# Kernel optimization log

Hardware: AMD Instinct MI355X
Metric: run time of the kernel (lower is better)

## Reference

```python
import jax, jax.numpy as jnp
import numpy as np
import math

B, S, D, H = 2, 2048, 1024, 16
DK = D // H
EPS = 1e-5

def setup_inputs() -> dict:
    key = jax.random.key(0)
    ks = jax.random.split(key, 16)
    s = 0.02
    return {
        'query': jax.random.normal(ks[0], (B, S, D), jnp.float32),
        'key': jax.random.normal(ks[1], (B, S, D), jnp.float32),
        'value': jax.random.normal(ks[2], (B, S, D), jnp.float32),
        'mask': jax.random.randint(ks[3], (B, 1, S, S), 0, 2, jnp.int32),
        'market_context': jax.random.normal(ks[4], (B, D), jnp.float32),
        'Wq': jax.random.normal(ks[5], (D, D), jnp.float32) * s,
        'bq': jnp.zeros((D,), jnp.float32),
        'Wk': jax.random.normal(ks[6], (D, D), jnp.float32) * s,
        'bk': jnp.zeros((D,), jnp.float32),
        'Wv': jax.random.normal(ks[7], (D, D), jnp.float32) * s,
        'bv': jnp.zeros((D,), jnp.float32),
        'Wo': jax.random.normal(ks[8], (D, D), jnp.float32) * s,
        'bo': jnp.zeros((D,), jnp.float32),
        'Wc': jax.random.normal(ks[9], (D, D), jnp.float32) * s,
        'bc': jnp.zeros((D,), jnp.float32),
        'ln_g': jnp.ones((D,), jnp.float32),
        'ln_b': jnp.zeros((D,), jnp.float32),
    }

def reference(query, key, value, mask, market_context,
              Wq, bq, Wk, bk, Wv, bv, Wo, bo, Wc, bc, ln_g, ln_b):
    b, s, d = query.shape
    # QKV projections -> [B, H, S, DK]
    Q = (query @ Wq + bq).reshape(b, s, H, DK).transpose(0, 2, 1, 3)
    K = (key @ Wk + bk).reshape(b, s, H, DK).transpose(0, 2, 1, 3)
    V = (value @ Wv + bv).reshape(b, s, H, DK).transpose(0, 2, 1, 3)
    # market context -> per-head bias added to K (broadcast over sequence)
    ctx = (market_context @ Wc + bc).reshape(b, H, DK)
    K = K + ctx[:, :, None, :]
    scores = jnp.einsum('bhqd,bhkd->bhqk', Q, K) / math.sqrt(DK)
    scores = jnp.where(mask == 0, jnp.float32(-1e9), scores)
    attn = jax.nn.softmax(scores, axis=-1)  # dropout is identity in eval
    ctx2 = jnp.einsum('bhqk,bhkd->bhqd', attn, V)
    ctx2 = ctx2.transpose(0, 2, 1, 3).reshape(b, s, d)
    out = ctx2 @ Wo + bo
    x = out + query
    mu = jnp.mean(x, axis=-1, keepdims=True)
    var = jnp.mean((x - mu) ** 2, axis=-1, keepdims=True)
    return (x - mu) * jax.lax.rsqrt(var + EPS) * ln_g + ln_b
```

## Files before the change

### kernel.cpp

```cpp
#include <hip/hip_runtime.h>
#include <cstdint>

typedef unsigned short u16;
typedef __attribute__((ext_vector_type(8))) short s16x8;
typedef __attribute__((ext_vector_type(8))) unsigned short u16x8;
typedef __attribute__((ext_vector_type(4))) float f32x4;
typedef __attribute__((ext_vector_type(16))) float f32x16;
typedef __attribute__((ext_vector_type(2))) unsigned uint2v;
typedef __attribute__((ext_vector_type(4))) unsigned uint4v;

#define CKF 0.18033688011f

__device__ inline u16 f2bf(float f){
  union { float f; uint32_t u; } v; v.f = f;
  uint32_t r = v.u + 0x7fffu + ((v.u >> 16) & 1u);
  return (u16)(r >> 16);
}

__device__ inline f32x4 mfma16(s16x8 a, s16x8 b, f32x4 c){
  return __builtin_amdgcn_mfma_f32_16x16x32_bf16(a, b, c, 0, 0, 0);
}
__device__ inline f32x16 mfma32(s16x8 a, s16x8 b, f32x16 c){
  return __builtin_amdgcn_mfma_f32_32x32x16_bf16(a, b, c, 0, 0, 0);
}
__device__ inline unsigned cvtpk(float a, float b){
  unsigned r;
  asm("v_cvt_pk_bf16_f32 %0, %1, %2" : "=v"(r) : "v"(a), "v"(b));
  return r;
}
__device__ inline float exp2a(float x){
  float r;
  asm("v_exp_f32 %0, %1" : "=v"(r) : "v"(x));
  return r;
}
__device__ inline void glds16(const u16* g, u16* l){
  __builtin_amdgcn_global_load_lds((const __attribute__((address_space(1))) void*)g,
                                   (__attribute__((address_space(3))) void*)l, 16, 0, 0);
}
__device__ inline void glds4(const unsigned* g, unsigned* l){
  __builtin_amdgcn_global_load_lds((const __attribute__((address_space(1))) void*)g,
                                   (__attribute__((address_space(3))) void*)l, 4, 0, 0);
}

struct PrepParams {
  const float* q; const float* k; const float* v;
  const int* mask; const float* mc;
  const float* W0; const float* W1; const float* W2; const float* W3;
  const float* Wc;
  u16* qo; u16* ko; u16* vo;
  u16* T0; u16* T1; u16* T2; u16* T3;
  unsigned* bits; float* part;
};

__global__ __launch_bounds__(256) void prep_kernel(PrepParams PP){
  __shared__ float shf[1056];
  int blk = blockIdx.x, tid = threadIdx.x;
  if (blk < 6144){
    int byy = blk >> 11, bxx = blk & 2047;
    const float* src = (byy == 0) ? PP.q : (byy == 1) ? PP.k : PP.v;
    u16* dst = (byy == 0) ? PP.qo : (byy == 1) ? PP.ko : PP.vo;
    size_t i = ((size_t)bxx * 256 + tid) * 8;
    float4 a = *(const float4*)(src + i);
    float4 b = *(const float4*)(src + i + 4);
    u16x8 o = { f2bf(a.x), f2bf(a.y), f2bf(a.z), f2bf(a.w),
                f2bf(b.x), f2bf(b.y), f2bf(b.z), f2bf(b.w) };
    *(u16x8*)(dst + i) = o;
  } else if (blk < 10240){
    int idx = blk - 6144;
    int bxx = idx & 31, byy = (idx >> 5) & 31, bzz = idx >> 10;
    const float* W = (bzz == 0) ? PP.W0 : (bzz == 1) ? PP.W1 : (bzz == 2) ? PP.W2 : PP.W3;
    u16* T = (bzz == 0) ? PP.T0 : (bzz == 1) ? PP.T1 : (bzz == 2) ? PP.T2 : PP.T3;
    float (*t)[33] = (float(*)[33])shf;
    int n0 = bxx * 32, k0 = byy * 32;
    int tx = tid & 31, ty = tid >> 5;
    #pragma unroll
    for (int j = 0; j < 4; j++)
      t[ty + j*8][tx] = W[(size_t)(k0 + ty + j*8) * 1024 + n0 + tx];
    __syncthreads();
    #pragma unroll
    for (int j = 0; j < 4; j++)
      T[(size_t)(n0 + ty + j*8) * 1024 + k0 + tx] = f2bf(t[tx][ty + j*8]);
  } else if (blk < 43008){
    size_t i = (size_t)(blk - 10240) * 256 + tid;
    int v = PP.mask[i];
    unsigned long long bal = __ballot(v != 0);
    int lane = tid & 63;
    if (lane == 0)       PP.bits[i >> 5] = (unsigned)bal;
    else if (lane == 32) PP.bits[i >> 5] = (unsigned)(bal >> 32);
  } else {
    int slice = blk - 43008;
    int k0 = slice * 64;
    float4 a0 = {0.f,0.f,0.f,0.f}, a1 = {0.f,0.f,0.f,0.f};
    const float* wp = PP.Wc + (size_t)k0 * 1024 + tid * 4;
    #pragma unroll 8
    for (int k = 0; k < 64; k++){
      float4 wv = *(const float4*)(wp + (size_t)k * 1024);
      float m0 = PP.mc[k0 + k], m1 = PP.mc[1024 + k0 + k];
      a0.x += m0 * wv.x; a0.y += m0 * wv.y; a0.z += m0 * wv.z; a0.w += m0 * wv.w;
      a1.x += m1 * wv.x; a1.y += m1 * wv.y; a1.z += m1 * wv.z; a1.w += m1 * wv.w;
    }
    *(float4*)(PP.part + ((size_t)slice * 2 + 0) * 1024 + tid * 4) = a0;
    *(float4*)(PP.part + ((size_t)slice * 2 + 1) * 1024 + tid * 4) = a1;
  }
}

__global__ __launch_bounds__(256) void ctxred_kernel(const float* __restrict__ part,
                                                     const float* __restrict__ bc,
                                                     float* __restrict__ ctx){
  int b = blockIdx.x, tid = threadIdx.x;
  float4 s = *(const float4*)(bc + tid * 4);
  #pragma unroll 4
  for (int sl = 0; sl < 16; sl++){
    float4 p = *(const float4*)(part + ((size_t)sl * 2 + b) * 1024 + tid * 4);
    s.x += p.x; s.y += p.y; s.z += p.z; s.w += p.w;
  }
  *(float4*)(ctx + (size_t)b * 1024 + tid * 4) = s;
}

struct GemmParams {
  const u16* A0; const u16* A1; const u16* A2; const u16* A3;
  const u16* W0; const u16* W1; const u16* W2; const u16* W3;
  const float* b0; const float* b1; const float* b2;
  const float* ctx;
  u16* outQ; u16* outK; u16* outV; float* outX0; float* outX1;
  int which;
};

__global__ __launch_bounds__(256, 2) void gemm_kernel(GemmParams P){
  int o = blockIdx.x + (blockIdx.y << 2) + (blockIdx.z << 7);
  int xcd = o & 7, j = o >> 3;
  int by = xcd + ((j & 3) << 3);
  int bx = (j >> 2) & 3;
  int bz = j >> 4;

  int z, kbase, nkt;
  const u16* A; const u16* W;
  if (P.which < 0){
    z = bz; kbase = 0; nkt = 32;
    if (z == 0){ A = P.A0; W = P.W0; }
    else if (z == 1){ A = P.A1; W = P.W1; }
    else { A = P.A2; W = P.W2; }
  } else {
    z = 3; kbase = bz * 512; nkt = 16;
    A = P.A3; W = P.W3;
  }
  int m0 = by * 128, n0 = bx * 256;
  __shared__ __align__(16) u16 sm[24576];
  int tid = threadIdx.x, lane = tid & 63, w = tid >> 6;
  int li = lane & 15, lq = lane >> 4;
  int wm = w >> 1, wn = w & 1;
  f32x4 zero = {0.f, 0.f, 0.f, 0.f};
  f32x4 acc[4][8];
  #pragma unroll
  for (int i = 0; i < 4; i++)
    #pragma unroll
    for (int jj = 0; jj < 8; jj++) acc[i][jj] = zero;

  int scolS = ((lane & 3) ^ ((lane >> 3) & 3)) << 3;
  int rowS = w * 16 + (lane >> 2);
  const u16* aS0 = A + (size_t)(m0 + rowS) * 1024 + kbase + scolS;
  const u16* aS1 = aS0 + (size_t)64 * 1024;
  const u16* bS0 = W + (size_t)(n0 + rowS) * 1024 + kbase + scolS;
  const u16* bS1 = bS0 + (size_t)64 * 1024;
  const u16* bS2 = bS0 + (size_t)128 * 1024;
  const u16* bS3 = bS0 + (size_t)192 * 1024;
  int d0 = (w * 64) * 8, d1 = (256 + w * 64) * 8;
  int d2 = (512 + w * 64) * 8, d3 = (768 + w * 64) * 8;

  int aOff[4], bOff[8];
  #pragma unroll
  for (int mb = 0; mb < 4; mb++){
    int row = wm * 64 + mb * 16 + li;
    aOff[mb] = (row * 32 + ((lq ^ ((row >> 1) & 3)) << 3)) * 2;
  }
  #pragma unroll
  for (int nb = 0; nb < 8; nb++){
    int row = wn * 128 + nb * 16 + li;
    bOff[nb] = 8192 + (row * 32 + ((lq ^ ((row >> 1) & 3)) << 3)) * 2;
  }

  auto STAGE = [&](int ct){
    u16* Ab = &sm[ct * 12288];
    u16* Bb = &sm[ct * 12288 + 4096];
    glds16(aS0, Ab + d0);
    glds16(aS1, Ab + d1);
    glds16(bS0, Bb + d0);
    glds16(bS1, Bb + d1);
    glds16(bS2, Bb + d2);
    glds16(bS3, Bb + d3);
  };
  auto ADV = [&](){ aS0 += 32; aS1 += 32; bS0 += 32; bS1 += 32; bS2 += 32; bS3 += 32; };

  auto KITER = [&](int kt, int ct){
    __builtin_amdgcn_s_barrier();
    if (kt + 1 < nkt){
      STAGE(ct ^ 1); ADV();
      asm volatile("s_waitcnt vmcnt(6)" ::: "memory");
    } else {
      asm volatile("s_waitcnt vmcnt(0)" ::: "memory");
    }
    __builtin_amdgcn_sched_barrier(0);
    __builtin_amdgcn_s_barrier();
    const char* base = (const char*)sm + ct * 24576;
    s16x8 af[4], bfr[8];
    #pragma unroll
    for (int mb = 0; mb < 4; mb++) af[mb] = *(const s16x8*)(base + aOff[mb]);
    #pragma unroll
    for (int nb = 0; nb < 8; nb++) bfr[nb] = *(const s16x8*)(base + bOff[nb]);
    __builtin_amdgcn_s_setprio(1);
    #pragma unroll
    for (int mb = 0; mb < 4; mb++)
      #pragma unroll
      for (int nb = 0; nb < 8; nb++)
        acc[mb][nb] = mfma16(af[mb], bfr[nb], acc[mb][nb]);
    __builtin_amdgcn_s_setprio(0);
  };

  STAGE(0); ADV();
  for (int kt = 0; kt < nkt; kt += 2){
    KITER(kt, 0);
    KITER(kt + 1, 1);
  }

  if (z == 2){
    const float* bias = P.b2;
    int bq_ = m0 >> 11, srow0 = m0 & 2047;
    u16* Ot = sm;
    #pragma unroll
    for (int h2 = 0; h2 < 2; h2++){
      __syncthreads();
      if (wn == h2){
        #pragma unroll
        for (int mb = 0; mb < 4; mb++){
          #pragma unroll
          for (int nb = 0; nb < 8; nb++){
            int cl = nb * 16 + li;
            int rowB = wm * 64 + mb * 16 + lq * 4;
            float bcol = bias[n0 + h2 * 128 + cl];
            unsigned p01 = cvtpk(acc[mb][nb][0] + bcol, acc[mb][nb][1] + bcol);
            unsigned p23 = cvtpk(acc[mb][nb][2] + bcol, acc[mb][nb][3] + bcol);
            int ba = cl * 256 + ((rowB * 2) ^ ((cl & 7) << 4));
            *(unsigned*)((char*)Ot + ba) = p01;
            *(unsigned*)((char*)Ot + ba + 4) = p23;
          }
        }
      }
      __syncthreads();
      #pragma unroll
      for (int i = 0; i < 8; i++){
        int u = i * 256 + tid;
        int cl = u >> 4, sc = u & 15;
        int ba = cl * 256 + ((sc * 16) ^ ((cl & 7) << 4));
        u16x8 vv = *(const u16x8*)((char*)Ot + ba);
        *(u16x8*)(P.outV + (((size_t)(bq_ * 1024 + n0 + h2 * 128 + cl)) << 11) + srow0 + sc * 8) = vv;
      }
    }
    return;
  }

  if (z == 3){
    float* Xo = (kbase == 0) ? P.outX0 : P.outX1;
    #pragma unroll
    for (int mb = 0; mb < 4; mb++){
      #pragma unroll
      for (int nb = 0; nb < 8; nb++){
        int col = n0 + wn * 128 + nb * 16 + li;
        #pragma unroll
        for (int r = 0; r < 4; r++){
          int row = m0 + wm * 64 + mb * 16 + lq * 4 + r;
          Xo[(size_t)row * 1024 + col] = acc[mb][nb][r];
        }
      }
    }
    return;
  }

  const float* bias = (z == 0) ? P.b0 : P.b1;
  #pragma unroll
  for (int mb = 0; mb < 4; mb++){
    #pragma unroll
    for (int nb = 0; nb < 8; nb++){
      int colL = wn * 128 + nb * 16 + li; int col = n0 + colL;
      float bcol = bias[col];
      #pragma unroll
      for (int r = 0; r < 4; r++){
        int row = m0 + wm * 64 + mb * 16 + lq * 4 + r;
        float v = acc[mb][nb][r] + bcol;
        if (z == 0){
          P.outQ[(size_t)row * 1024 + col] = f2bf(v * CKF);
        } else {
          v += P.ctx[(size_t)(row >> 11) * 1024 + col];
          P.outK[(size_t)row * 1024 + col] = f2bf(v);
        }
      }
    }
  }
}

__global__ __launch_bounds__(256) void attn_kernel(
    const u16* __restrict__ Qg, const u16* __restrict__ Kg, const u16* __restrict__ Vtg,
    const unsigned* __restrict__ mbits, u16* __restrict__ ctx2){
  __shared__ __align__(16) u16 arena[17408];
  int tid = threadIdx.x, lane = tid & 63, w = tid >> 6;
  int l31 = lane & 31, hi = lane >> 5;
  int r7 = l31 & 7;
  int orig = blockIdx.x + (blockIdx.y << 4);
  int swz = (orig & 7) * 64 + (orig >> 3);
  int q0 = (swz & 15) * 128, bh = swz >> 4, b = bh >> 4, h = bh & 15;

  s16x8 qf[4];
  {
    const u16* qp = Qg + (size_t)(b * 2048 + q0 + w * 32 + l31) * 1024 + h * 64 + hi * 8;
    #pragma unroll
    for (int ks = 0; ks < 4; ks++)
      qf[ks] = *(const s16x8*)(qp + ks * 16);
  }
  s16x8 onesf;
  #pragma unroll
  for (int e = 0; e < 8; e++) onesf[e] = (short)0x3F80;
  f32x16 ZERO;
  #pragma unroll
  for (int r = 0; r < 16; r++) ZERO[r] = 0.f;

  int scolS = ((lane & 7) ^ (lane >> 3)) << 3;
  int rowS = w * 16 + (lane >> 3);
  const u16* kS0 = Kg + (size_t)(b * 2048 + rowS) * 1024 + h * 64 + scolS;
  const u16* kS1 = kS0 + (size_t)8 * 1024;
  const u16* vS0 = Vtg + (((size_t)(bh * 64 + rowS)) << 11) + scolS;
  const u16* vS1 = vS0 + ((size_t)8 << 11);
  int um = w * 64 + lane;
  const unsigned* mS = mbits + (size_t)(b * 2048 + q0 + (um >> 1)) * 64 + (um & 1);
  int kD0 = w * 1024, kD1 = w * 1024 + 512;

  int qr = w * 32 + l31;
  int koff[2][4], voff[2][4];
  #pragma unroll
  for (int jj = 0; jj < 2; jj++)
    #pragma unroll
    for (int ks = 0; ks < 4; ks++){
      koff[jj][ks] = ((jj * 32 + l31) * 64 + (((ks * 2 + hi) ^ r7) << 3)) * 2;
      voff[jj][ks] = 8192 + ((jj * 32 + l31) * 64 + (((ks * 2 + hi) ^ r7) << 3)) * 2;
    }
  int mB = 32768 + qr * 8;

  auto STAGE = [&](int ct){
    u16* dst = &arena[ct * 8192];
    glds16(kS0, dst + kD0);
    glds16(kS1, dst + kD1);
    glds16(vS0, dst + 4096 + kD0);
    glds16(vS1, dst + 4096 + kD1);
    glds4(mS, (unsigned*)&arena[16384] + ct * 256 + w * 64);
  };
  auto ADV = [&](){
    kS0 += (size_t)64 * 1024; kS1 += (size_t)64 * 1024;
    vS0 += 64; vS1 += 64; mS += 2;
  };

  f32x16 accO[2], accS;
  #pragma unroll
  for (int d = 0; d < 2; d++) accO[d] = ZERO;
  accS = ZERO;

  STAGE(0); ADV();

  auto ITER = [&](int t, int ct){
    __builtin_amdgcn_s_barrier();
    if (t < 31){
      STAGE(ct ^ 1); ADV();
      asm volatile("s_waitcnt vmcnt(5)" ::: "memory");
    } else {
      asm volatile("s_waitcnt vmcnt(0)" ::: "memory");
    }
    __builtin_amdgcn_sched_barrier(0);
    __builtin_amdgcn_s_barrier();
    const char* base = (const char*)arena + ct * 16384;

    f32x16 S[2];
    __builtin_amdgcn_s_setprio(1);
    #pragma unroll
    for (int jj = 0; jj < 2; jj++){
      S[jj] = ZERO;
      #pragma unroll
      for (int ks = 0; ks < 4; ks++){
        s16x8 kf = *(const s16x8*)(base + koff[jj][ks]);
        S[jj] = mfma32(kf, qf[ks], S[jj]);
      }
    }
    __builtin_amdgcn_s_setprio(0);

    uint2v mw = *(const uint2v*)((const char*)arena + ct * 1024 + mB);
    unsigned mh0 = mw[0] >> (hi << 2), mh1 = mw[1] >> (hi << 2);
    #pragma unroll
    for (int jj = 0; jj < 2; jj++){
      unsigned mh = jj ? mh1 : mh0;
      #pragma unroll
      for (int rg = 0; rg < 16; rg++){
        int pos = (rg & 3) + ((rg >> 2) << 3);
        float pv = exp2a(S[jj][rg]);
        S[jj][rg] = ((mh >> pos) & 1u) ? pv : 0.f;
      }
    }

    s16x8 pf[4];
    #pragma unroll
    for (int jj = 0; jj < 2; jj++){
      #pragma unroll
      for (int hs = 0; hs < 2; hs++){
        int rb = hs * 8;
        unsigned A0 = cvtpk(S[jj][rb + 0], S[jj][rb + 1]);
        unsigned A1 = cvtpk(S[jj][rb + 2], S[jj][rb + 3]);
        unsigned B0 = cvtpk(S[jj][rb + 4], S[jj][rb + 5]);
        unsigned B1 = cvtpk(S[jj][rb + 6], S[jj][rb + 7]);
        uint2v r01 = __builtin_amdgcn_permlane32_swap(A0, B0, false, false);
        uint2v r23 = __builtin_amdgcn_permlane32_swap(A1, B1, false, false);
        uint4v uu = { r01[0], r23[0], r01[1], r23[1] };
        pf[jj * 2 + hs] = *(s16x8*)&uu;
      }
    }
    __builtin_amdgcn_s_setprio(1);
    #pragma unroll
    for (int c = 0; c < 4; c++){
      #pragma unroll
      for (int dh = 0; dh < 2; dh++){
        s16x8 vf = *(const s16x8*)(base + voff[dh][c]);
        accO[dh] = mfma32(vf, pf[c], accO[dh]);
      }
      accS = mfma32(onesf, pf[c], accS);
    }
    __builtin_amdgcn_s_setprio(0);
  };

  for (int t = 0; t < 32; t += 2){
    ITER(t, 0);
    ITER(t + 1, 1);
  }

  __syncthreads();
  float lsum = accS[0];
  float inv = 1.f / lsum;
  u16* Ot = arena;
  #pragma unroll
  for (int dh = 0; dh < 2; dh++){
    #pragma unroll
    for (int rg = 0; rg < 16; rg += 2){
      int dk = dh * 32 + (rg & 3) + ((rg >> 2) << 3) + (hi << 2);
      unsigned pk = cvtpk(accO[dh][rg] * inv, accO[dh][rg + 1] * inv);
      *(unsigned*)&Ot[qr * 64 + (((dk >> 3) ^ (qr & 7)) << 3) + (dk & 7)] = pk;
    }
  }
  __syncthreads();
  #pragma unroll
  for (int i = 0; i < 4; i++){
    int u = i * 256 + tid, row = u >> 3, slot = u & 7;
    u16x8 vv = *(const u16x8*)&Ot[row * 64 + ((slot ^ (row & 7)) << 3)];
    *(u16x8*)(ctx2 + (size_t)(b * 2048 + q0 + row) * 1024 + h * 64 + slot * 8) = vv;
  }
}

__global__ __launch_bounds__(256) void ln_kernel(const float* __restrict__ X0,
                                                 const float* __restrict__ X1,
                                                 const float* __restrict__ qres,
                                                 const float* __restrict__ bo,
                                                 const float* __restrict__ g,
                                                 const float* __restrict__ bb,
                                                 float* __restrict__ out){
  size_t row = blockIdx.x;
  int tid = threadIdx.x;
  float4 a = *(const float4*)(X0 + row * 1024 + tid * 4);
  float4 c = *(const float4*)(X1 + row * 1024 + tid * 4);
  float4 q = *(const float4*)(qres + row * 1024 + tid * 4);
  float4 bv = *(const float4*)(bo + tid * 4);
  float4 v;
  v.x = a.x + c.x + q.x + bv.x;
  v.y = a.y + c.y + q.y + bv.y;
  v.z = a.z + c.z + q.z + bv.z;
  v.w = a.w + c.w + q.w + bv.w;
  float s = v.x + v.y + v.z + v.w;
  float s2 = v.x*v.x + v.y*v.y + v.z*v.z + v.w*v.w;
  #pragma unroll
  for (int o = 1; o < 64; o <<= 1){
    s += __shfl_xor(s, o, 64);
    s2 += __shfl_xor(s2, o, 64);
  }
  __shared__ float rs[4], rs2[4];
  int w = tid >> 6;
  if ((tid & 63) == 0){ rs[w] = s; rs2[w] = s2; }
  __syncthreads();
  s = rs[0] + rs[1] + rs[2] + rs[3];
  s2 = rs2[0] + rs2[1] + rs2[2] + rs2[3];
  float mu = s * (1.f / 1024.f);
  float var = s2 * (1.f / 1024.f) - mu * mu;
  float rstd = rsqrtf(var + 1e-5f);
  float4 gg = *(const float4*)(g + tid * 4);
  float4 bt = *(const float4*)(bb + tid * 4);
  float4 o;
  o.x = (v.x - mu) * rstd * gg.x + bt.x;
  o.y = (v.y - mu) * rstd * gg.y + bt.y;
  o.z = (v.z - mu) * rstd * gg.z + bt.z;
  o.w = (v.w - mu) * rstd * gg.w + bt.w;
  *(float4*)(out + row * 1024 + tid * 4) = o;
}

extern "C" void kernel_launch(void* const* d_in, const int* in_sizes, int n_in,
                              void* d_out, int out_size, void* d_ws, size_t ws_size,
                              hipStream_t stream){
  const float* query = (const float*)d_in[0];
  const float* key_  = (const float*)d_in[1];
  const float* value = (const float*)d_in[2];
  const int*   mask  = (const int*)d_in[3];
  const float* mc    = (const float*)d_in[4];
  const float* Wq = (const float*)d_in[5];  const float* bq = (const float*)d_in[6];
  const float* Wk = (const float*)d_in[7];  const float* bk = (const float*)d_in[8];
  const float* Wv = (const float*)d_in[9];  const float* bv = (const float*)d_in[10];
  const float* Wo = (const float*)d_in[11]; const float* bo = (const float*)d_in[12];
  const float* Wc = (const float*)d_in[13]; const float* bc = (const float*)d_in[14];
  const float* lng = (const float*)d_in[15]; const float* lnb = (const float*)d_in[16];
  float* outp = (float*)d_out;
  uint8_t* ws = (uint8_t*)d_ws;
  const size_t MB = (size_t)1 << 20;
  if (ws_size < 58 * MB) return;

  u16* q_bf = (u16*)(ws + 0);
  u16* k_bf = (u16*)(ws + 8 * MB);
  u16* v_bf = (u16*)(ws + 16 * MB);
  float* X0 = (float*)(ws + 8 * MB);
  u16* Qb   = (u16*)(ws + 24 * MB);
  u16* Kb   = (u16*)(ws + 32 * MB);
  float* X1 = (float*)(ws + 32 * MB);
  u16* Vt   = (u16*)(ws + 40 * MB);
  u16* Wqt  = (u16*)(ws + 48 * MB);
  u16* Wkt  = (u16*)(ws + 50 * MB);
  u16* Wvt  = (u16*)(ws + 52 * MB);
  u16* Wot  = (u16*)(ws + 54 * MB);
  unsigned* mbits = (unsigned*)(ws + 56 * MB);
  float* ctxf = (float*)(ws + 57 * MB);
  float* ctxpart = (float*)(ws + 57 * MB + 65536);
  u16* ctx2 = q_bf;

  PrepParams PP;
  PP.q = query; PP.k = key_; PP.v = value; PP.mask = mask; PP.mc = mc;
  PP.W0 = Wq; PP.W1 = Wk; PP.W2 = Wv; PP.W3 = Wo; PP.Wc = Wc;
  PP.qo = q_bf; PP.ko = k_bf; PP.vo = v_bf;
  PP.T0 = Wqt; PP.T1 = Wkt; PP.T2 = Wvt; PP.T3 = Wot;
  PP.bits = mbits; PP.part = ctxpart;
  prep_kernel<<<43024, 256, 0, stream>>>(PP);

  ctxred_kernel<<<2, 256, 0, stream>>>(ctxpart, bc, ctxf);

  GemmParams gp;
  gp.A0 = q_bf; gp.A1 = k_bf; gp.A2 = v_bf; gp.A3 = ctx2;
  gp.W0 = Wqt;  gp.W1 = Wkt;  gp.W2 = Wvt;  gp.W3 = Wot;
  gp.b0 = bq;   gp.b1 = bk;   gp.b2 = bv;
  gp.ctx = ctxf;
  gp.outQ = Qb; gp.outK = Kb; gp.outV = Vt; gp.outX0 = X0; gp.outX1 = X1;
  gp.which = -1;
  gemm_kernel<<<dim3(4, 32, 3), 256, 0, stream>>>(gp);

  attn_kernel<<<dim3(16, 32), 256, 0, stream>>>(Qb, Kb, Vt, mbits, ctx2);

  gp.which = 3;
  gemm_kernel<<<dim3(4, 32, 2), 256, 0, stream>>>(gp);

  ln_kernel<<<4096, 256, 0, stream>>>(X0, X1, query, bo, lng, lnb, outp);
}
```

Measured before the change: 161.1 us.

## Halve GEMM N-tile and split attention key range across two wave groups

The GEMM tile shrinks from 128x256 to 128x128, doubling the grid (8x32 blocks per z) and cutting LDS and accumulator use per block. The attention kernel goes to 512 threads: two wave groups each process half of the key sequence with their own double-buffered LDS staging. Their partial outputs and row sums are then merged through LDS before normalization. This targets occupancy and latency hiding on the many CUs, in exchange for more global traffic in the GEMMs, a larger LDS footprint in attention and an extra reduction step.

```diff
diff --git a/kernel.cpp b/kernel.cpp
--- a/kernel.cpp
+++ b/kernel.cpp
@@ -126,12 +126,12 @@
   int which;
 };
 
-__global__ __launch_bounds__(256, 2) void gemm_kernel(GemmParams P){
-  int o = blockIdx.x + (blockIdx.y << 2) + (blockIdx.z << 7);
+__global__ __launch_bounds__(256) void gemm_kernel(GemmParams P){
+  int o = blockIdx.x + (blockIdx.y << 3) + (blockIdx.z << 8);
   int xcd = o & 7, j = o >> 3;
   int by = xcd + ((j & 3) << 3);
-  int bx = (j >> 2) & 3;
-  int bz = j >> 4;
+  int bx = (j >> 2) & 7;
+  int bz = j >> 5;
 
   int z, kbase, nkt;
   const u16* A; const u16* W;
@@ -144,74 +144,69 @@
     z = 3; kbase = bz * 512; nkt = 16;
     A = P.A3; W = P.W3;
   }
-  int m0 = by * 128, n0 = bx * 256;
-  __shared__ __align__(16) u16 sm[24576];
+  int m0 = by * 128, n0 = bx * 128;
+  __shared__ __align__(16) u16 sm[16384];
   int tid = threadIdx.x, lane = tid & 63, w = tid >> 6;
   int li = lane & 15, lq = lane >> 4;
   int wm = w >> 1, wn = w & 1;
   f32x4 zero = {0.f, 0.f, 0.f, 0.f};
-  f32x4 acc[4][8];
+  f32x4 acc[4][4];
   #pragma unroll
   for (int i = 0; i < 4; i++)
     #pragma unroll
-    for (int jj = 0; jj < 8; jj++) acc[i][jj] = zero;
+    for (int jj = 0; jj < 4; jj++) acc[i][jj] = zero;
 
   int scolS = ((lane & 3) ^ ((lane >> 3) & 3)) << 3;
-  int rowS = w * 16 + (lane >> 2);
-  const u16* aS0 = A + (size_t)(m0 + rowS) * 1024 + kbase + scolS;
+  int row0 = w * 16 + (lane >> 2);
+  const u16* aS0 = A + (size_t)(m0 + row0) * 1024 + kbase + scolS;
   const u16* aS1 = aS0 + (size_t)64 * 1024;
-  const u16* bS0 = W + (size_t)(n0 + rowS) * 1024 + kbase + scolS;
+  const u16* bS0 = W + (size_t)(n0 + row0) * 1024 + kbase + scolS;
   const u16* bS1 = bS0 + (size_t)64 * 1024;
-  const u16* bS2 = bS0 + (size_t)128 * 1024;
-  const u16* bS3 = bS0 + (size_t)192 * 1024;
-  int d0 = (w * 64) * 8, d1 = (256 + w * 64) * 8;
-  int d2 = (512 + w * 64) * 8, d3 = (768 + w * 64) * 8;
-
-  int aOff[4], bOff[8];
+  int aD0 = (w * 64) * 8, aD1 = (256 + w * 64) * 8;
+
+  int aOff[4], bOff[4];
   #pragma unroll
   for (int mb = 0; mb < 4; mb++){
     int row = wm * 64 + mb * 16 + li;
     aOff[mb] = (row * 32 + ((lq ^ ((row >> 1) & 3)) << 3)) * 2;
   }
   #pragma unroll
-  for (int nb = 0; nb < 8; nb++){
-    int row = wn * 128 + nb * 16 + li;
+  for (int nb = 0; nb < 4; nb++){
+    int row = wn * 64 + nb * 16 + li;
     bOff[nb] = 8192 + (row * 32 + ((lq ^ ((row >> 1) & 3)) << 3)) * 2;
   }
 
   auto STAGE = [&](int ct){
-    u16* Ab = &sm[ct * 12288];
-    u16* Bb = &sm[ct * 12288 + 4096];
-    glds16(aS0, Ab + d0);
-    glds16(aS1, Ab + d1);
-    glds16(bS0, Bb + d0);
-    glds16(bS1, Bb + d1);
-    glds16(bS2, Bb + d2);
-    glds16(bS3, Bb + d3);
+    u16* Ab = &sm[ct * 8192];
+    u16* Bb = &sm[ct * 8192 + 4096];
+    glds16(aS0, Ab + aD0);
+    glds16(aS1, Ab + aD1);
+    glds16(bS0, Bb + aD0);
+    glds16(bS1, Bb + aD1);
   };
-  auto ADV = [&](){ aS0 += 32; aS1 += 32; bS0 += 32; bS1 += 32; bS2 += 32; bS3 += 32; };
+  auto ADV = [&](){ aS0 += 32; aS1 += 32; bS0 += 32; bS1 += 32; };
 
   auto KITER = [&](int kt, int ct){
     __builtin_amdgcn_s_barrier();
     if (kt + 1 < nkt){
       STAGE(ct ^ 1); ADV();
-      asm volatile("s_waitcnt vmcnt(6)" ::: "memory");
+      asm volatile("s_waitcnt vmcnt(4)" ::: "memory");
     } else {
       asm volatile("s_waitcnt vmcnt(0)" ::: "memory");
     }
     __builtin_amdgcn_sched_barrier(0);
     __builtin_amdgcn_s_barrier();
-    const char* base = (const char*)sm + ct * 24576;
-    s16x8 af[4], bfr[8];
+    const char* base = (const char*)sm + ct * 16384;
+    s16x8 af[4], bfr[4];
     #pragma unroll
     for (int mb = 0; mb < 4; mb++) af[mb] = *(const s16x8*)(base + aOff[mb]);
     #pragma unroll
-    for (int nb = 0; nb < 8; nb++) bfr[nb] = *(const s16x8*)(base + bOff[nb]);
+    for (int nb = 0; nb < 4; nb++) bfr[nb] = *(const s16x8*)(base + bOff[nb]);
     __builtin_amdgcn_s_setprio(1);
     #pragma unroll
     for (int mb = 0; mb < 4; mb++)
       #pragma unroll
-      for (int nb = 0; nb < 8; nb++)
+      for (int nb = 0; nb < 4; nb++)
         acc[mb][nb] = mfma16(af[mb], bfr[nb], acc[mb][nb]);
     __builtin_amdgcn_s_setprio(0);
   };
@@ -224,36 +219,31 @@
 
   if (z == 2){
     const float* bias = P.b2;
+    __syncthreads();
+    u16* Ot = sm;
+    #pragma unroll
+    for (int mb = 0; mb < 4; mb++){
+      #pragma unroll
+      for (int nb = 0; nb < 4; nb++){
+        int colL = wn * 64 + nb * 16 + li;
+        int rowB = wm * 64 + mb * 16 + lq * 4;
+        float bcol = bias[n0 + colL];
+        unsigned p01 = cvtpk(acc[mb][nb][0] + bcol, acc[mb][nb][1] + bcol);
+        unsigned p23 = cvtpk(acc[mb][nb][2] + bcol, acc[mb][nb][3] + bcol);
+        int ba = colL * 256 + ((rowB * 2) ^ ((colL & 7) << 4));
+        *(unsigned*)((char*)Ot + ba) = p01;
+        *(unsigned*)((char*)Ot + ba + 4) = p23;
+      }
+    }
+    __syncthreads();
     int bq_ = m0 >> 11, srow0 = m0 & 2047;
-    u16* Ot = sm;
-    #pragma unroll
-    for (int h2 = 0; h2 < 2; h2++){
-      __syncthreads();
-      if (wn == h2){
-        #pragma unroll
-        for (int mb = 0; mb < 4; mb++){
-          #pragma unroll
-          for (int nb = 0; nb < 8; nb++){
-            int cl = nb * 16 + li;
-            int rowB = wm * 64 + mb * 16 + lq * 4;
-            float bcol = bias[n0 + h2 * 128 + cl];
-            unsigned p01 = cvtpk(acc[mb][nb][0] + bcol, acc[mb][nb][1] + bcol);
-            unsigned p23 = cvtpk(acc[mb][nb][2] + bcol, acc[mb][nb][3] + bcol);
-            int ba = cl * 256 + ((rowB * 2) ^ ((cl & 7) << 4));
-            *(unsigned*)((char*)Ot + ba) = p01;
-            *(unsigned*)((char*)Ot + ba + 4) = p23;
-          }
-        }
-      }
-      __syncthreads();
-      #pragma unroll
-      for (int i = 0; i < 8; i++){
-        int u = i * 256 + tid;
-        int cl = u >> 4, sc = u & 15;
-        int ba = cl * 256 + ((sc * 16) ^ ((cl & 7) << 4));
-        u16x8 vv = *(const u16x8*)((char*)Ot + ba);
-        *(u16x8*)(P.outV + (((size_t)(bq_ * 1024 + n0 + h2 * 128 + cl)) << 11) + srow0 + sc * 8) = vv;
-      }
+    #pragma unroll
+    for (int i = 0; i < 8; i++){
+      int u = i * 256 + tid;
+      int colL = u >> 4, sc = u & 15;
+      int ba = colL * 256 + ((sc * 16) ^ ((colL & 7) << 4));
+      u16x8 vv = *(const u16x8*)((char*)Ot + ba);
+      *(u16x8*)(P.outV + (((size_t)(bq_ * 1024 + n0 + colL)) << 11) + srow0 + sc * 8) = vv;
     }
     return;
   }
@@ -263,8 +253,8 @@
     #pragma unroll
     for (int mb = 0; mb < 4; mb++){
       #pragma unroll
-      for (int nb = 0; nb < 8; nb++){
-        int col = n0 + wn * 128 + nb * 16 + li;
+      for (int nb = 0; nb < 4; nb++){
+        int col = n0 + wn * 64 + nb * 16 + li;
         #pragma unroll
         for (int r = 0; r < 4; r++){
           int row = m0 + wm * 64 + mb * 16 + lq * 4 + r;
@@ -279,8 +269,8 @@
   #pragma unroll
   for (int mb = 0; mb < 4; mb++){
     #pragma unroll
-    for (int nb = 0; nb < 8; nb++){
-      int colL = wn * 128 + nb * 16 + li; int col = n0 + colL;
+    for (int nb = 0; nb < 4; nb++){
+      int colL = wn * 64 + nb * 16 + li; int col = n0 + colL;
       float bcol = bias[col];
       #pragma unroll
       for (int r = 0; r < 4; r++){
@@ -297,20 +287,22 @@
   }
 }
 
-__global__ __launch_bounds__(256) void attn_kernel(
+__global__ __launch_bounds__(512) void attn_kernel(
     const u16* __restrict__ Qg, const u16* __restrict__ Kg, const u16* __restrict__ Vtg,
     const unsigned* __restrict__ mbits, u16* __restrict__ ctx2){
-  __shared__ __align__(16) u16 arena[17408];
+  __shared__ __align__(16) u16 arena[36864];
   int tid = threadIdx.x, lane = tid & 63, w = tid >> 6;
+  int qw = w & 3, p = w >> 2;
   int l31 = lane & 31, hi = lane >> 5;
   int r7 = l31 & 7;
   int orig = blockIdx.x + (blockIdx.y << 4);
   int swz = (orig & 7) * 64 + (orig >> 3);
   int q0 = (swz & 15) * 128, bh = swz >> 4, b = bh >> 4, h = bh & 15;
+  int qr = qw * 32 + l31;
 
   s16x8 qf[4];
   {
-    const u16* qp = Qg + (size_t)(b * 2048 + q0 + w * 32 + l31) * 1024 + h * 64 + hi * 8;
+    const u16* qp = Qg + (size_t)(b * 2048 + q0 + qr) * 1024 + h * 64 + hi * 8;
     #pragma unroll
     for (int ks = 0; ks < 4; ks++)
       qf[ks] = *(const s16x8*)(qp + ks * 16);
@@ -323,16 +315,15 @@
   for (int r = 0; r < 16; r++) ZERO[r] = 0.f;
 
   int scolS = ((lane & 7) ^ (lane >> 3)) << 3;
-  int rowS = w * 16 + (lane >> 3);
-  const u16* kS0 = Kg + (size_t)(b * 2048 + rowS) * 1024 + h * 64 + scolS;
+  int rowS = qw * 16 + (lane >> 3);
+  const u16* kS0 = Kg + (size_t)(b * 2048 + p * 64 + rowS) * 1024 + h * 64 + scolS;
   const u16* kS1 = kS0 + (size_t)8 * 1024;
-  const u16* vS0 = Vtg + (((size_t)(bh * 64 + rowS)) << 11) + scolS;
+  const u16* vS0 = Vtg + (((size_t)(bh * 64 + rowS)) << 11) + p * 64 + scolS;
   const u16* vS1 = vS0 + ((size_t)8 << 11);
-  int um = w * 64 + lane;
-  const unsigned* mS = mbits + (size_t)(b * 2048 + q0 + (um >> 1)) * 64 + (um & 1);
-  int kD0 = w * 1024, kD1 = w * 1024 + 512;
-
-  int qr = w * 32 + l31;
+  int um = qw * 64 + lane;
+  const unsigned* mS = mbits + (size_t)(b * 2048 + q0 + (um >> 1)) * 64 + p * 2 + (um & 1);
+  int kD0 = qw * 1024, kD1 = qw * 1024 + 512;
+
   int koff[2][4], voff[2][4];
   #pragma unroll
   for (int jj = 0; jj < 2; jj++)
@@ -341,19 +332,20 @@
       koff[jj][ks] = ((jj * 32 + l31) * 64 + (((ks * 2 + hi) ^ r7) << 3)) * 2;
       voff[jj][ks] = 8192 + ((jj * 32 + l31) * 64 + (((ks * 2 + hi) ^ r7) << 3)) * 2;
     }
-  int mB = 32768 + qr * 8;
+  const char* baseP = (const char*)arena + p * 32768;
+  int mBp = 65536 + p * 2048 + qr * 8;
 
   auto STAGE = [&](int ct){
-    u16* dst = &arena[ct * 8192];
+    u16* dst = &arena[(p * 2 + ct) * 8192];
     glds16(kS0, dst + kD0);
     glds16(kS1, dst + kD1);
     glds16(vS0, dst + 4096 + kD0);
     glds16(vS1, dst + 4096 + kD1);
-    glds4(mS, (unsigned*)&arena[16384] + ct * 256 + w * 64);
+    glds4(mS, (unsigned*)&arena[32768] + (p * 2 + ct) * 256 + qw * 64);
   };
   auto ADV = [&](){
-    kS0 += (size_t)64 * 1024; kS1 += (size_t)64 * 1024;
-    vS0 += 64; vS1 += 64; mS += 2;
+    kS0 += (size_t)128 * 1024; kS1 += (size_t)128 * 1024;
+    vS0 += 128; vS1 += 128; mS += 4;
   };
 
   f32x16 accO[2], accS;
@@ -363,9 +355,9 @@
 
   STAGE(0); ADV();
 
-  auto ITER = [&](int t, int ct){
+  auto ITER = [&](int jt, int ct){
     __builtin_amdgcn_s_barrier();
-    if (t < 31){
+    if (jt < 15){
       STAGE(ct ^ 1); ADV();
       asm volatile("s_waitcnt vmcnt(5)" ::: "memory");
     } else {
@@ -373,7 +365,7 @@
     }
     __builtin_amdgcn_sched_barrier(0);
     __builtin_amdgcn_s_barrier();
-    const char* base = (const char*)arena + ct * 16384;
+    const char* base = baseP + ct * 16384;
 
     f32x16 S[2];
     __builtin_amdgcn_s_setprio(1);
@@ -388,7 +380,7 @@
     }
     __builtin_amdgcn_s_setprio(0);
 
-    uint2v mw = *(const uint2v*)((const char*)arena + ct * 1024 + mB);
+    uint2v mw = *(const uint2v*)((const char*)arena + mBp + ct * 1024);
     unsigned mh0 = mw[0] >> (hi << 2), mh1 = mw[1] >> (hi << 2);
     #pragma unroll
     for (int jj = 0; jj < 2; jj++){
@@ -430,28 +422,47 @@
     __builtin_amdgcn_s_setprio(0);
   };
 
-  for (int t = 0; t < 32; t += 2){
-    ITER(t, 0);
-    ITER(t + 1, 1);
+  for (int jt = 0; jt < 16; jt += 2){
+    ITER(jt, 0);
+    ITER(jt + 1, 1);
   }
 
   __syncthreads();
   float lsum = accS[0];
-  float inv = 1.f / lsum;
-  u16* Ot = arena;
-  #pragma unroll
-  for (int dh = 0; dh < 2; dh++){
-    #pragma unroll
-    for (int rg = 0; rg < 16; rg += 2){
-      int dk = dh * 32 + (rg & 3) + ((rg >> 2) << 3) + (hi << 2);
-      unsigned pk = cvtpk(accO[dh][rg] * inv, accO[dh][rg + 1] * inv);
-      *(unsigned*)&Ot[qr * 64 + (((dk >> 3) ^ (qr & 7)) << 3) + (dk & 7)] = pk;
-    }
+  float* mg = (float*)arena;
+  int li33 = (qw * 64 + lane) * 33;
+  if (p == 1){
+    #pragma unroll
+    for (int dh = 0; dh < 2; dh++)
+      #pragma unroll
+      for (int rg = 0; rg < 16; rg++)
+        mg[li33 + dh * 16 + rg] = accO[dh][rg];
+    mg[li33 + 32] = lsum;
   }
   __syncthreads();
-  #pragma unroll
-  for (int i = 0; i < 4; i++){
-    int u = i * 256 + tid, row = u >> 3, slot = u & 7;
+  u16* Ot = &arena[28672];
+  if (p == 0){
+    #pragma unroll
+    for (int dh = 0; dh < 2; dh++)
+      #pragma unroll
+      for (int rg = 0; rg < 16; rg++)
+        accO[dh][rg] += mg[li33 + dh * 16 + rg];
+    lsum += mg[li33 + 32];
+    float inv = 1.f / lsum;
+    #pragma unroll
+    for (int dh = 0; dh < 2; dh++){
+      #pragma unroll
+      for (int rg = 0; rg < 16; rg += 2){
+        int dk = dh * 32 + (rg & 3) + ((rg >> 2) << 3) + (hi << 2);
+        unsigned pk = cvtpk(accO[dh][rg] * inv, accO[dh][rg + 1] * inv);
+        *(unsigned*)&Ot[qr * 64 + (((dk >> 3) ^ (qr & 7)) << 3) + (dk & 7)] = pk;
+      }
+    }
+  }
+  __syncthreads();
+  #pragma unroll
+  for (int i = 0; i < 2; i++){
+    int u = i * 512 + tid, row = u >> 3, slot = u & 7;
     u16x8 vv = *(const u16x8*)&Ot[row * 64 + ((slot ^ (row & 7)) << 3)];
     *(u16x8*)(ctx2 + (size_t)(b * 2048 + q0 + row) * 1024 + h * 64 + slot * 8) = vv;
   }
@@ -554,12 +565,12 @@
   gp.ctx = ctxf;
   gp.outQ = Qb; gp.outK = Kb; gp.outV = Vt; gp.outX0 = X0; gp.outX1 = X1;
   gp.which = -1;
-  gemm_kernel<<<dim3(4, 32, 3), 256, 0, stream>>>(gp);
-
-  attn_kernel<<<dim3(16, 32), 256, 0, stream>>>(Qb, Kb, Vt, mbits, ctx2);
+  gemm_kernel<<<dim3(8, 32, 3), 256, 0, stream>>>(gp);
+
+  attn_kernel<<<dim3(16, 32), 512, 0, stream>>>(Qb, Kb, Vt, mbits, ctx2);
 
   gp.which = 3;
-  gemm_kernel<<<dim3(4, 32, 2), 256, 0, stream>>>(gp);
+  gemm_kernel<<<dim3(8, 32, 2), 256, 0, stream>>>(gp);
 
   ln_kernel<<<4096, 256, 0, stream>>>(X0, X1, query, bo, lng, lnb, outp);
 }
```

Result: no change. 160.9 us (-0.1%).
